# Optimization experiments

Measured on AMD Instinct MI355X. Metric: run time of the kernel, lower is better.

The kernel has to match this reference:

```python
import jax, jax.numpy as jnp
import numpy as np

EMBED = 768
HEADS = 12
HEAD_DIM = EMBED // HEADS
HIDDEN = 3072
EPS = 1e-5


def setup_inputs() -> dict:
    key = jax.random.key(0)
    ks = jax.random.split(key, 8)
    s = lambda d: 1.0 / np.sqrt(d)
    return {
        "x": jax.random.normal(ks[0], (1, 4096, EMBED), jnp.float32),
        "ln1_w": jnp.ones((EMBED,), jnp.float32),
        "ln1_b": jnp.zeros((EMBED,), jnp.float32),
        "qkv_w": jax.random.normal(ks[1], (3 * EMBED, EMBED), jnp.float32) * s(EMBED),
        "qkv_b": jnp.zeros((3 * EMBED,), jnp.float32),
        "out_w": jax.random.normal(ks[2], (EMBED, EMBED), jnp.float32) * s(EMBED),
        "out_b": jnp.zeros((EMBED,), jnp.float32),
        "ln2_w": jnp.ones((EMBED,), jnp.float32),
        "ln2_b": jnp.zeros((EMBED,), jnp.float32),
        "fc1_w": jax.random.normal(ks[3], (HIDDEN, EMBED), jnp.float32) * s(EMBED),
        "fc1_b": jnp.zeros((HIDDEN,), jnp.float32),
        "fc2_w": jax.random.normal(ks[4], (EMBED, HIDDEN), jnp.float32) * s(HIDDEN),
        "fc2_b": jnp.zeros((EMBED,), jnp.float32),
    }


def _layernorm(x, w, b):
    mu = jnp.mean(x, axis=-1, keepdims=True)
    var = jnp.mean(jnp.square(x - mu), axis=-1, keepdims=True)
    return (x - mu) * jax.lax.rsqrt(var + EPS) * w + b


def reference(x, ln1_w, ln1_b, qkv_w, qkv_b, out_w, out_b,
              ln2_w, ln2_b, fc1_w, fc1_b, fc2_w, fc2_b):
    B, N, _ = x.shape
    # attention branch
    h = _layernorm(x, ln1_w, ln1_b)
    qkv = h @ qkv_w.T + qkv_b                      # [B,N,3E]
    qkv = qkv.reshape(B, N, 3, HEADS, HEAD_DIM)
    q = jnp.transpose(qkv[:, :, 0], (0, 2, 1, 3))  # [B,H,N,D]
    k = jnp.transpose(qkv[:, :, 1], (0, 2, 1, 3))
    v = jnp.transpose(qkv[:, :, 2], (0, 2, 1, 3))
    scores = jnp.einsum("bhqd,bhkd->bhqk", q, k) / np.sqrt(HEAD_DIM)
    probs = jax.nn.softmax(scores, axis=-1)
    attn = jnp.einsum("bhqk,bhkd->bhqd", probs, v)
    attn = jnp.transpose(attn, (0, 2, 1, 3)).reshape(B, N, EMBED)
    x = x + (attn @ out_w.T + out_b)
    # mlp branch
    h = _layernorm(x, ln2_w, ln2_b)
    h = jax.nn.gelu(h @ fc1_w.T + fc1_b, approximate=False)
    x = x + (h @ fc2_w.T + fc2_b)
    return x
```

## Files before the change

kernel.cpp:

```cpp
#include <hip/hip_runtime.h>
#include <hip/hip_bf16.h>

#define SEQ  4096
#define EMB  768
#define NH   12
#define HD   64
#define HID  3072
#define QKVC 2304

typedef __attribute__((ext_vector_type(8))) short bf16x8;
typedef __attribute__((ext_vector_type(4))) float f32x4;

#define MFMA16(a,b,c) __builtin_amdgcn_mfma_f32_16x16x32_bf16(a,b,c,0,0,0)

#define QSCL 0.18033688f

__device__ __forceinline__ unsigned short f2bf(float f){
  union { float f; unsigned u; } c; c.f = f;
  unsigned r = c.u + 0x7FFFu + ((c.u >> 16) & 1u);
  return (unsigned short)(r >> 16);
}

__device__ __forceinline__ float bf2f(unsigned short u){
  union { unsigned u; float f; } c; c.u = (unsigned)u << 16; return c.f;
}

__device__ __forceinline__ unsigned cvtpk(float a, float b){
  unsigned r;
  asm("v_cvt_pk_bf16_f32 %0, %1, %2" : "=v"(r) : "v"(a), "v"(b));
  return r;
}

__device__ __forceinline__ void gload_lds16(const unsigned short* g, unsigned short* l){
  __builtin_amdgcn_global_load_lds(
      (const __attribute__((address_space(1))) unsigned int*)g,
      (__attribute__((address_space(3))) unsigned int*)l, 16, 0, 0);
}

__global__ void cvt4_kernel(const float* __restrict__ s0, unsigned short* __restrict__ d0, int n0,
                            const float* __restrict__ s1, unsigned short* __restrict__ d1, int n1,
                            const float* __restrict__ s2, unsigned short* __restrict__ d2, int n2,
                            const float* __restrict__ s3, unsigned short* __restrict__ d3, int n3){
  long e = ((long)blockIdx.x * 256 + threadIdx.x) << 2;
  const float* s; unsigned short* d;
  if (e < n0){ s = s0; d = d0; }
  else if ((e -= n0) < n1){ s = s1; d = d1; }
  else if ((e -= n1) < n2){ s = s2; d = d2; }
  else if ((e -= n2) < n3){ s = s3; d = d3; }
  else return;
  float4 v = *(const float4*)(s + e);
  ushort4 u;
  u.x = f2bf(v.x); u.y = f2bf(v.y); u.z = f2bf(v.z); u.w = f2bf(v.w);
  *(ushort4*)(d + e) = u;
}

__global__ __launch_bounds__(256) void ln_kernel(const float* __restrict__ x,
    const float* __restrict__ w, const float* __restrict__ b,
    unsigned short* __restrict__ out)
{
  const int row = blockIdx.x;
  const float* xr = x + (size_t)row * EMB;
  const int t = threadIdx.x;
  float v0 = xr[t], v1 = xr[t + 256], v2 = xr[t + 512];
  float s  = v0 + v1 + v2;
  float s2 = v0*v0 + v1*v1 + v2*v2;
  #pragma unroll
  for (int off = 32; off; off >>= 1){ s += __shfl_down(s, off); s2 += __shfl_down(s2, off); }
  __shared__ float rs[4], rq[4], st[2];
  int wv = t >> 6;
  if ((t & 63) == 0){ rs[wv] = s; rq[wv] = s2; }
  __syncthreads();
  if (t == 0){
    float S  = rs[0] + rs[1] + rs[2] + rs[3];
    float S2 = rq[0] + rq[1] + rq[2] + rq[3];
    float mu  = S * (1.f / 768.f);
    float var = S2 * (1.f / 768.f) - mu * mu;
    st[0] = mu; st[1] = rsqrtf(var + 1e-5f);
  }
  __syncthreads();
  float mu = st[0], rstd = st[1];
  unsigned short* orow = out + (size_t)row * EMB;
  orow[t]       = f2bf((v0 - mu) * rstd * w[t]       + b[t]);
  orow[t + 256] = f2bf((v1 - mu) * rstd * w[t + 256] + b[t + 256]);
  orow[t + 512] = f2bf((v2 - mu) * rstd * w[t + 512] + b[t + 512]);
}

template<int EPI, int BM, int BN, int DBUF>
__global__ __launch_bounds__(256, 3) void gemm_kernel(
    const unsigned short* __restrict__ A, const unsigned short* __restrict__ B,
    const float* __restrict__ bias, const float* __restrict__ res,
    unsigned short* __restrict__ Ob, float* __restrict__ Of,
    int M, int N, int K)
{
  constexpr int MF = BM / 32;
  constexpr int NF = BN / 32;
  constexpr int NB = DBUF ? 2 : 1;
  __shared__ unsigned short sA[NB][BM * 64];
  __shared__ unsigned short sB[NB][BN * 64];
  const int tid  = threadIdx.x;
  const int w    = tid >> 6, lane = tid & 63;
  const int wr   = w >> 1,   wc   = w & 1;
  const int l15  = lane & 15, l4  = lane >> 4;
  const int tm   = blockIdx.y, tn = blockIdx.x;
  const unsigned short* Ab = A + (size_t)tm * BM * K;
  const unsigned short* Bb = B + (size_t)tn * BN * K;

  f32x4 acc[MF][NF];
  #pragma unroll
  for (int m = 0; m < MF; ++m)
    #pragma unroll
    for (int n = 0; n < NF; ++n){ acc[m][n][0]=0.f; acc[m][n][1]=0.f; acc[m][n][2]=0.f; acc[m][n][3]=0.f; }

  #define GSTAGE(buf, kt) { \
    const int k0_ = (kt) << 6; \
    _Pragma("unroll") \
    for (int i = 0; i < MF; ++i){ \
      int c = i * 256 + tid; int row = c >> 3; int skc = (c & 7) ^ (row & 7); \
      gload_lds16(Ab + (size_t)row * K + k0_ + skc * 8, &sA[buf][(i * 256 + w * 64) * 8]); } \
    _Pragma("unroll") \
    for (int i = 0; i < NF; ++i){ \
      int c = i * 256 + tid; int row = c >> 3; int skc = (c & 7) ^ (row & 7); \
      gload_lds16(Bb + (size_t)row * K + k0_ + skc * 8, &sB[buf][(i * 256 + w * 64) * 8]); }}

  #define GCOMPUTE(buf) { \
    _Pragma("unroll") \
    for (int ks = 0; ks < 2; ++ks){ \
      bf16x8 af[MF], bg[NF]; \
      _Pragma("unroll") \
      for (int m = 0; m < MF; ++m){ \
        int row = wr * (BM / 2) + m * 16 + l15; \
        int kc  = ks * 4 + l4; \
        af[m] = *(const bf16x8*)&sA[buf][row * 64 + ((kc ^ (row & 7)) << 3)]; } \
      _Pragma("unroll") \
      for (int n = 0; n < NF; ++n){ \
        int row = wc * (BN / 2) + n * 16 + l15; \
        int kc  = ks * 4 + l4; \
        bg[n] = *(const bf16x8*)&sB[buf][row * 64 + ((kc ^ (row & 7)) << 3)]; } \
      _Pragma("unroll") \
      for (int m = 0; m < MF; ++m) \
        _Pragma("unroll") \
        for (int n = 0; n < NF; ++n) \
          acc[m][n] = MFMA16(af[m], bg[n], acc[m][n]); }}

  const int nk = K >> 6;
  if (DBUF){
    GSTAGE(0, 0);
    int cur = 0;
    for (int kt = 0; kt < nk; ++kt){
      __syncthreads();
      if (kt + 1 < nk) GSTAGE(cur ^ 1, kt + 1);
      GCOMPUTE(cur % NB);
      cur ^= 1;
    }
  } else {
    for (int kt = 0; kt < nk; ++kt){
      GSTAGE(0, kt);
      __syncthreads();
      GCOMPUTE(0);
      __syncthreads();
    }
  }
  #undef GSTAGE
  #undef GCOMPUTE

  #pragma unroll
  for (int m = 0; m < MF; ++m){
    int row0 = tm * BM + wr * (BM / 2) + m * 16 + l4 * 4;
    #pragma unroll
    for (int n = 0; n < NF; ++n){
      int col = tn * BN + wc * (BN / 2) + n * 16 + l15;
      float bv = bias[col];
      #pragma unroll
      for (int r = 0; r < 4; ++r){
        int row = row0 + r;
        float v = acc[m][n][r] + bv;
        if (EPI == 0){
          Ob[(size_t)row * N + col] = f2bf(v);
        } else if (EPI == 1){
          v = 0.5f * v * (1.f + erff(v * 0.70710678118f));
          Ob[(size_t)row * N + col] = f2bf(v);
        } else if (EPI == 3){
          if (col < EMB) v *= QSCL;
          Ob[(size_t)row * N + col] = f2bf(v);
        } else {
          v += res[(size_t)row * N + col];
          Of[(size_t)row * N + col] = v;
        }
      }
    }
  }
}

__global__ __launch_bounds__(256, 3) void attn_kernel(
    const unsigned short* __restrict__ qkv,
    unsigned short* __restrict__ pO, float2* __restrict__ pml)
{
  __shared__ unsigned short sK[2][64 * 64];
  __shared__ unsigned short sVt[2][64 * 64];
  __shared__ unsigned short sEp[4][16 * 72];
  const int tid = threadIdx.x, w = tid >> 6, lane = tid & 63;
  const int l15 = lane & 15, l4 = lane >> 4;

  const int bid  = blockIdx.x;
  const int v_id = (bid & 7) * 96 + (bid >> 3);
  const int head = v_id >> 6;
  const int r6   = v_id & 63;
  const int qt   = r6 >> 1;
  const int sk   = r6 & 1;

  const int koff = EMB + head * HD;
  const int voff = 2 * EMB + head * HD;
  const int qbase = qt * 128 + w * 32;
  const int tbase = sk * 32;

  bf16x8 qf[2][2];
  #pragma unroll
  for (int qg = 0; qg < 2; ++qg){
    const unsigned short* qp = qkv + (size_t)(qbase + qg * 16 + l15) * QKVC + head * HD + l4 * 8;
    qf[qg][0] = *(const bf16x8*)qp;
    qf[qg][1] = *(const bf16x8*)(qp + 32);
  }

  f32x4 oaccT[4][2];
  #pragma unroll
  for (int i = 0; i < 4; ++i)
    #pragma unroll
    for (int qg = 0; qg < 2; ++qg){ oaccT[i][qg][0]=0.f; oaccT[i][qg][1]=0.f; oaccT[i][qg][2]=0.f; oaccT[i][qg][3]=0.f; }
  float m0 = -3.0e38f, m1 = -3.0e38f, l0 = 0.f, l1 = 0.f;

  const int krow = tid >> 3;
  const int kskc = (tid & 7) ^ (krow & 7);
  const int vp_  = tid >> 3;
  const int d0   = (tid & 7) * 8;
  const int w16  = vp_ & 15;
  const int qpos = (w16 & 1) | (((w16 >> 3) & 1) << 1) | (((w16 >> 1) & 3) << 2);
  const int Pc   = ((vp_ >> 4) << 2) | (qpos >> 2);
  const int Ps   = qpos & 3;

  #define KSTAGE(buf, t) { \
    const int kv0_ = (t) << 6; \
    gload_lds16(qkv + (size_t)(kv0_ + krow) * QKVC + koff + kskc * 8,      &sK[buf][(w * 64) * 8]); \
    gload_lds16(qkv + (size_t)(kv0_ + 32 + krow) * QKVC + koff + kskc * 8, &sK[buf][(256 + w * 64) * 8]); }

  #define VLOAD(t) { \
    const unsigned short* vp = qkv + (size_t)(((t) << 6) + vp_ * 2) * QKVC + voff + d0; \
    va = *(const bf16x8*)vp; \
    vb = *(const bf16x8*)(vp + QKVC); }

  #define VCOMMIT(buf) { \
    _Pragma("unroll") \
    for (int i = 0; i < 8; ++i){ \
      unsigned pk = (unsigned)(unsigned short)va[i] | ((unsigned)(unsigned short)vb[i] << 16); \
      *(unsigned*)&sVt[buf][(d0 + i) * 64 + ((Pc ^ (tid & 7) ^ i) << 3) + Ps * 2] = pk; \
    } }

  bf16x8 va, vb;
  KSTAGE(0, tbase);
  VLOAD(tbase);
  VCOMMIT(0);

  for (int tt = 0; tt < 32; ++tt){
    const int cur = tt & 1;
    __syncthreads();
    const bool pre = (tt < 31);
    if (pre){
      KSTAGE(cur ^ 1, tbase + tt + 1);
      VLOAD(tbase + tt + 1);
    }

    f32x4 sf[4][2];
    #pragma unroll
    for (int i = 0; i < 4; ++i)
      #pragma unroll
      for (int qg = 0; qg < 2; ++qg){ sf[i][qg][0]=0.f; sf[i][qg][1]=0.f; sf[i][qg][2]=0.f; sf[i][qg][3]=0.f; }
    __builtin_amdgcn_s_setprio(1);
    #pragma unroll
    for (int ks = 0; ks < 2; ++ks){
      bf16x8 kf[4];
      #pragma unroll
      for (int nb = 0; nb < 4; ++nb){
        int row = 16 * nb + l15;
        kf[nb] = *(const bf16x8*)&sK[cur][(row * 8 + ((4 * ks + l4) ^ (row & 7))) * 8];
      }
      #pragma unroll
      for (int nb = 0; nb < 4; ++nb){
        sf[nb][0] = MFMA16(kf[nb], qf[0][ks], sf[nb][0]);
        sf[nb][1] = MFMA16(kf[nb], qf[1][ks], sf[nb][1]);
      }
    }
    __builtin_amdgcn_s_setprio(0);

    float mx0, mx1;
    {
      float a = sf[0][0][0], b = sf[0][1][0];
      #pragma unroll
      for (int nb = 0; nb < 4; ++nb)
        #pragma unroll
        for (int r = 0; r < 4; ++r){
          a = fmaxf(a, sf[nb][0][r]);
          b = fmaxf(b, sf[nb][1][r]);
        }
      a = fmaxf(a, __shfl_xor(a, 16)); a = fmaxf(a, __shfl_xor(a, 32));
      b = fmaxf(b, __shfl_xor(b, 16)); b = fmaxf(b, __shfl_xor(b, 32));
      mx0 = a; mx1 = b;
    }
    bool ok = (mx0 <= m0 + 8.f) && (mx1 <= m1 + 8.f);
    if (!__all(ok)){
      float nm0 = fmaxf(m0, mx0), nm1 = fmaxf(m1, mx1);
      float c0 = __builtin_amdgcn_exp2f(m0 - nm0);
      float c1 = __builtin_amdgcn_exp2f(m1 - nm1);
      m0 = nm0; m1 = nm1; l0 *= c0; l1 *= c1;
      #pragma unroll
      for (int db = 0; db < 4; ++db)
        #pragma unroll
        for (int r = 0; r < 4; ++r){ oaccT[db][0][r] *= c0; oaccT[db][1][r] *= c1; }
    }
    unsigned pbw[2][2][4];
    {
      float ps0 = 0.f, ps1 = 0.f;
      #pragma unroll
      for (int nb = 0; nb < 4; ++nb){
        float p0[4], p1[4];
        #pragma unroll
        for (int r = 0; r < 4; ++r){
          p0[r] = __builtin_amdgcn_exp2f(sf[nb][0][r] - m0); ps0 += p0[r];
          p1[r] = __builtin_amdgcn_exp2f(sf[nb][1][r] - m1); ps1 += p1[r];
        }
        pbw[0][nb >> 1][(nb & 1) * 2]     = cvtpk(p0[0], p0[1]);
        pbw[0][nb >> 1][(nb & 1) * 2 + 1] = cvtpk(p0[2], p0[3]);
        pbw[1][nb >> 1][(nb & 1) * 2]     = cvtpk(p1[0], p1[1]);
        pbw[1][nb >> 1][(nb & 1) * 2 + 1] = cvtpk(p1[2], p1[3]);
      }
      ps0 += __shfl_xor(ps0, 16); ps0 += __shfl_xor(ps0, 32);
      ps1 += __shfl_xor(ps1, 16); ps1 += __shfl_xor(ps1, 32);
      l0 += ps0; l1 += ps1;
    }

    __builtin_amdgcn_s_setprio(1);
    {
      bf16x8 vv[2][4];
      #pragma unroll
      for (int ks = 0; ks < 2; ++ks)
        #pragma unroll
        for (int db = 0; db < 4; ++db){
          int d = 16 * db + l15;
          int cp = (4 * ks + l4) ^ ((d >> 3) & 7) ^ (d & 7);
          vv[ks][db] = *(const bf16x8*)&sVt[cur][d * 64 + cp * 8];
        }
      union { unsigned uw[4]; bf16x8 v; } pb;
      #pragma unroll
      for (int qg = 0; qg < 2; ++qg){
        bf16x8 pb0, pb1;
        pb.uw[0]=pbw[qg][0][0]; pb.uw[1]=pbw[qg][0][1]; pb.uw[2]=pbw[qg][0][2]; pb.uw[3]=pbw[qg][0][3]; pb0 = pb.v;
        pb.uw[0]=pbw[qg][1][0]; pb.uw[1]=pbw[qg][1][1]; pb.uw[2]=pbw[qg][1][2]; pb.uw[3]=pbw[qg][1][3]; pb1 = pb.v;
        #pragma unroll
        for (int db = 0; db < 4; ++db){
          oaccT[db][qg] = MFMA16(vv[0][db], pb0, oaccT[db][qg]);
          oaccT[db][qg] = MFMA16(vv[1][db], pb1, oaccT[db][qg]);
        }
      }
    }
    __builtin_amdgcn_s_setprio(0);

    if (pre) VCOMMIT(cur ^ 1);
  }

  #pragma unroll
  for (int qg = 0; qg < 2; ++qg){
    unsigned short* sPw = sEp[w];
    #pragma unroll
    for (int db = 0; db < 4; ++db)
      #pragma unroll
      for (int dw = 0; dw < 2; ++dw){
        unsigned pk = cvtpk(oaccT[db][qg][2 * dw], oaccT[db][qg][2 * dw + 1]);
        *(unsigned*)&sPw[l15 * 72 + 16 * db + 4 * l4 + 2 * dw] = pk;
      }
    int qe = lane >> 2, de = (lane & 3) * 16;
    bf16x8 r0 = *(const bf16x8*)&sPw[qe * 72 + de];
    bf16x8 r1 = *(const bf16x8*)&sPw[qe * 72 + de + 8];
    unsigned short* op = pO + ((size_t)(sk * NH + head) * SEQ + qbase + qg * 16 + qe) * 64 + de;
    *(bf16x8*)op = r0;
    *(bf16x8*)(op + 8) = r1;
  }
  if (lane < 16){
    size_t r = (size_t)(sk * NH + head) * SEQ + qbase + l15;
    pml[r]      = make_float2(m0, l0);
    pml[r + 16] = make_float2(m1, l1);
  }
  #undef KSTAGE
  #undef VLOAD
  #undef VCOMMIT
}

__global__ __launch_bounds__(256) void comb_kernel(
    const unsigned short* __restrict__ pO, const float2* __restrict__ pml,
    unsigned short* __restrict__ o)
{
  const int t = threadIdx.x;
  const int row = blockIdx.x * 64 + (t >> 2);
  const int dseg = (t & 3) * 16;
  float2 a = pml[row], b = pml[NH * SEQ + row];
  float M = fmaxf(a.x, b.x);
  float c0 = __builtin_amdgcn_exp2f(a.x - M);
  float c1 = __builtin_amdgcn_exp2f(b.x - M);
  float inv = 1.f / (c0 * a.y + c1 * b.y);
  c0 *= inv; c1 *= inv;
  const unsigned short* p0 = pO + (size_t)row * 64 + dseg;
  const unsigned short* p1 = p0 + (size_t)NH * SEQ * 64;
  bf16x8 x0 = *(const bf16x8*)p0, x1 = *(const bf16x8*)(p0 + 8);
  bf16x8 y0 = *(const bf16x8*)p1, y1 = *(const bf16x8*)(p1 + 8);
  const int head = row >> 12, q = row & (SEQ - 1);
  unsigned short* op = o + (size_t)q * EMB + head * HD + dseg;
  union { unsigned uw[4]; bf16x8 v; } r0, r1;
  #pragma unroll
  for (int i = 0; i < 4; ++i){
    r0.uw[i] = cvtpk(c0 * bf2f((unsigned short)x0[2*i])   + c1 * bf2f((unsigned short)y0[2*i]),
                     c0 * bf2f((unsigned short)x0[2*i+1]) + c1 * bf2f((unsigned short)y0[2*i+1]));
    r1.uw[i] = cvtpk(c0 * bf2f((unsigned short)x1[2*i])   + c1 * bf2f((unsigned short)y1[2*i]),
                     c0 * bf2f((unsigned short)x1[2*i+1]) + c1 * bf2f((unsigned short)y1[2*i+1]));
  }
  *(bf16x8*)op = r0.v;
  *(bf16x8*)(op + 8) = r1.v;
}

extern "C" void kernel_launch(void* const* d_in, const int* in_sizes, int n_in,
                              void* d_out, int out_size, void* d_ws, size_t ws_size,
                              hipStream_t stream)
{
  const float* x    = (const float*)d_in[0];
  const float* ln1w = (const float*)d_in[1];
  const float* ln1b = (const float*)d_in[2];
  const float* qkvw = (const float*)d_in[3];
  const float* qkvb = (const float*)d_in[4];
  const float* outw = (const float*)d_in[5];
  const float* outb = (const float*)d_in[6];
  const float* ln2w = (const float*)d_in[7];
  const float* ln2b = (const float*)d_in[8];
  const float* fc1w = (const float*)d_in[9];
  const float* fc1b = (const float*)d_in[10];
  const float* fc2w = (const float*)d_in[11];
  const float* fc2b = (const float*)d_in[12];
  float* out = (float*)d_out;

  char* ws = (char*)d_ws;
  unsigned short* wqkv = (unsigned short*)ws; ws += (size_t)QKVC * EMB * 2;
  unsigned short* wout = (unsigned short*)ws; ws += (size_t)EMB * EMB * 2;
  unsigned short* wfc1 = (unsigned short*)ws; ws += (size_t)HID * EMB * 2;
  unsigned short* wfc2 = (unsigned short*)ws; ws += (size_t)EMB * HID * 2;
  unsigned short* h1   = (unsigned short*)ws; ws += (size_t)SEQ * EMB * 2;
  unsigned short* qkv  = (unsigned short*)ws; ws += (size_t)SEQ * QKVC * 2;
  unsigned short* h3   = (unsigned short*)ws; ws += (size_t)SEQ * HID * 2;
  unsigned short* attnb = h1;
  unsigned short* h2    = qkv;
  unsigned short* pO  = h3;
  float2*         pml = (float2*)(h3 + (size_t)2 * NH * SEQ * 64);

  const int n0 = QKVC * EMB, n1 = EMB * EMB, n2 = HID * EMB, n3 = EMB * HID;
  cvt4_kernel<<<(n0 + n1 + n2 + n3) / 4 / 256, 256, 0, stream>>>(
      qkvw, wqkv, n0, outw, wout, n1, fc1w, wfc1, n2, fc2w, wfc2, n3);

  ln_kernel<<<SEQ, 256, 0, stream>>>(x, ln1w, ln1b, h1);

  gemm_kernel<3, 128, 128, 0><<<dim3(QKVC / 128, SEQ / 128), 256, 0, stream>>>(
      h1, wqkv, qkvb, nullptr, qkv, nullptr, SEQ, QKVC, EMB);

  attn_kernel<<<SEQ / 128 * NH * 2, 256, 0, stream>>>(qkv, pO, pml);
  comb_kernel<<<NH * SEQ / 64, 256, 0, stream>>>(pO, pml, attnb);

  gemm_kernel<2, 64, 64, 1><<<dim3(EMB / 64, SEQ / 64), 256, 0, stream>>>(
      attnb, wout, outb, x, nullptr, out, SEQ, EMB, EMB);

  ln_kernel<<<SEQ, 256, 0, stream>>>(out, ln2w, ln2b, h2);

  gemm_kernel<1, 128, 128, 0><<<dim3(HID / 128, SEQ / 128), 256, 0, stream>>>(
      h2, wfc1, fc1b, nullptr, h3, nullptr, SEQ, HID, EMB);

  gemm_kernel<2, 64, 64, 1><<<dim3(EMB / 64, SEQ / 64), 256, 0, stream>>>(
      h3, wfc2, fc2b, out, nullptr, out, SEQ, EMB, HID);
}
```

Before: 214.2 us.

## Double-buffer all GEMMs with templated K-tile and use fast sigmoid-form GELU

The GEMM kernel now takes the K-tile size as a template parameter and always double-buffers its shared-memory stages. The 128x128 QKV and FC1 GEMMs move from single-buffered BK=64 to double-buffered BK=32, keeping roughly the same LDS footprint while overlapping global-to-LDS loads with MFMA work. The 64x64 GEMMs get a higher occupancy hint in their launch bounds. The erf-based GELU epilogue is replaced with an exp2/rcp sigmoid-form tanh approximation, which is cheaper but differs slightly from exact GELU.

```diff
diff --git a/kernel.cpp b/kernel.cpp
--- a/kernel.cpp
+++ b/kernel.cpp
@@ -29,6 +29,12 @@
   unsigned r;
   asm("v_cvt_pk_bf16_f32 %0, %1, %2" : "=v"(r) : "v"(a), "v"(b));
   return r;
+}
+
+__device__ __forceinline__ float gelu_f(float x){
+  float x2 = x * x;
+  float u  = __builtin_amdgcn_exp2f(x * fmaf(x2, 0.1029433f, 2.3022082f));
+  return x * u * __builtin_amdgcn_rcpf(1.f + u);
 }
 
 __device__ __forceinline__ void gload_lds16(const unsigned short* g, unsigned short* l){
@@ -85,18 +91,21 @@
   orow[t + 512] = f2bf((v2 - mu) * rstd * w[t + 512] + b[t + 512]);
 }
 
-template<int EPI, int BM, int BN, int DBUF>
-__global__ __launch_bounds__(256, 3) void gemm_kernel(
+template<int EPI, int BM, int BN, int BK>
+__global__ __launch_bounds__(256, (BM == 64 ? 4 : 3)) void gemm_kernel(
     const unsigned short* __restrict__ A, const unsigned short* __restrict__ B,
     const float* __restrict__ bias, const float* __restrict__ res,
     unsigned short* __restrict__ Ob, float* __restrict__ Of,
     int M, int N, int K)
 {
-  constexpr int MF = BM / 32;
-  constexpr int NF = BN / 32;
-  constexpr int NB = DBUF ? 2 : 1;
-  __shared__ unsigned short sA[NB][BM * 64];
-  __shared__ unsigned short sB[NB][BN * 64];
+  constexpr int MF  = BM / 32;
+  constexpr int NF  = BN / 32;
+  constexpr int KS  = BK / 32;
+  constexpr int CPR = BK / 8;
+  constexpr int AIT = BM * BK / 2048;
+  constexpr int BIT = BN * BK / 2048;
+  __shared__ unsigned short sA[2][BM * BK];
+  __shared__ unsigned short sB[2][BN * BK];
   const int tid  = threadIdx.x;
   const int w    = tid >> 6, lane = tid & 63;
   const int wr   = w >> 1,   wc   = w & 1;
@@ -112,53 +121,44 @@
     for (int n = 0; n < NF; ++n){ acc[m][n][0]=0.f; acc[m][n][1]=0.f; acc[m][n][2]=0.f; acc[m][n][3]=0.f; }
 
   #define GSTAGE(buf, kt) { \
-    const int k0_ = (kt) << 6; \
+    const int k0_ = (kt) * BK; \
     _Pragma("unroll") \
-    for (int i = 0; i < MF; ++i){ \
-      int c = i * 256 + tid; int row = c >> 3; int skc = (c & 7) ^ (row & 7); \
+    for (int i = 0; i < AIT; ++i){ \
+      int c = i * 256 + tid; int row = c / CPR; int skc = (c % CPR) ^ (row & (CPR - 1)); \
       gload_lds16(Ab + (size_t)row * K + k0_ + skc * 8, &sA[buf][(i * 256 + w * 64) * 8]); } \
     _Pragma("unroll") \
-    for (int i = 0; i < NF; ++i){ \
-      int c = i * 256 + tid; int row = c >> 3; int skc = (c & 7) ^ (row & 7); \
+    for (int i = 0; i < BIT; ++i){ \
+      int c = i * 256 + tid; int row = c / CPR; int skc = (c % CPR) ^ (row & (CPR - 1)); \
       gload_lds16(Bb + (size_t)row * K + k0_ + skc * 8, &sB[buf][(i * 256 + w * 64) * 8]); }}
 
   #define GCOMPUTE(buf) { \
     _Pragma("unroll") \
-    for (int ks = 0; ks < 2; ++ks){ \
+    for (int ks = 0; ks < KS; ++ks){ \
       bf16x8 af[MF], bg[NF]; \
       _Pragma("unroll") \
       for (int m = 0; m < MF; ++m){ \
         int row = wr * (BM / 2) + m * 16 + l15; \
         int kc  = ks * 4 + l4; \
-        af[m] = *(const bf16x8*)&sA[buf][row * 64 + ((kc ^ (row & 7)) << 3)]; } \
+        af[m] = *(const bf16x8*)&sA[buf][row * BK + ((kc ^ (row & (CPR - 1))) << 3)]; } \
       _Pragma("unroll") \
       for (int n = 0; n < NF; ++n){ \
         int row = wc * (BN / 2) + n * 16 + l15; \
         int kc  = ks * 4 + l4; \
-        bg[n] = *(const bf16x8*)&sB[buf][row * 64 + ((kc ^ (row & 7)) << 3)]; } \
+        bg[n] = *(const bf16x8*)&sB[buf][row * BK + ((kc ^ (row & (CPR - 1))) << 3)]; } \
       _Pragma("unroll") \
       for (int m = 0; m < MF; ++m) \
         _Pragma("unroll") \
         for (int n = 0; n < NF; ++n) \
           acc[m][n] = MFMA16(af[m], bg[n], acc[m][n]); }}
 
-  const int nk = K >> 6;
-  if (DBUF){
-    GSTAGE(0, 0);
-    int cur = 0;
-    for (int kt = 0; kt < nk; ++kt){
-      __syncthreads();
-      if (kt + 1 < nk) GSTAGE(cur ^ 1, kt + 1);
-      GCOMPUTE(cur % NB);
-      cur ^= 1;
-    }
-  } else {
-    for (int kt = 0; kt < nk; ++kt){
-      GSTAGE(0, kt);
-      __syncthreads();
-      GCOMPUTE(0);
-      __syncthreads();
-    }
+  const int nk = K / BK;
+  GSTAGE(0, 0);
+  int cur = 0;
+  for (int kt = 0; kt < nk; ++kt){
+    __syncthreads();
+    if (kt + 1 < nk) GSTAGE(cur ^ 1, kt + 1);
+    GCOMPUTE(cur);
+    cur ^= 1;
   }
   #undef GSTAGE
   #undef GCOMPUTE
@@ -177,8 +177,7 @@
         if (EPI == 0){
           Ob[(size_t)row * N + col] = f2bf(v);
         } else if (EPI == 1){
-          v = 0.5f * v * (1.f + erff(v * 0.70710678118f));
-          Ob[(size_t)row * N + col] = f2bf(v);
+          Ob[(size_t)row * N + col] = f2bf(gelu_f(v));
         } else if (EPI == 3){
           if (col < EMB) v *= QSCL;
           Ob[(size_t)row * N + col] = f2bf(v);
@@ -461,20 +460,20 @@
 
   ln_kernel<<<SEQ, 256, 0, stream>>>(x, ln1w, ln1b, h1);
 
-  gemm_kernel<3, 128, 128, 0><<<dim3(QKVC / 128, SEQ / 128), 256, 0, stream>>>(
+  gemm_kernel<3, 128, 128, 32><<<dim3(QKVC / 128, SEQ / 128), 256, 0, stream>>>(
       h1, wqkv, qkvb, nullptr, qkv, nullptr, SEQ, QKVC, EMB);
 
   attn_kernel<<<SEQ / 128 * NH * 2, 256, 0, stream>>>(qkv, pO, pml);
   comb_kernel<<<NH * SEQ / 64, 256, 0, stream>>>(pO, pml, attnb);
 
-  gemm_kernel<2, 64, 64, 1><<<dim3(EMB / 64, SEQ / 64), 256, 0, stream>>>(
+  gemm_kernel<2, 64, 64, 64><<<dim3(EMB / 64, SEQ / 64), 256, 0, stream>>>(
       attnb, wout, outb, x, nullptr, out, SEQ, EMB, EMB);
 
   ln_kernel<<<SEQ, 256, 0, stream>>>(out, ln2w, ln2b, h2);
 
-  gemm_kernel<1, 128, 128, 0><<<dim3(HID / 128, SEQ / 128), 256, 0, stream>>>(
+  gemm_kernel<1, 128, 128, 32><<<dim3(HID / 128, SEQ / 128), 256, 0, stream>>>(
       h2, wfc1, fc1b, nullptr, h3, nullptr, SEQ, HID, EMB);
 
-  gemm_kernel<2, 64, 64, 1><<<dim3(EMB / 64, SEQ / 64), 256, 0, stream>>>(
+  gemm_kernel<2, 64, 64, 64><<<dim3(EMB / 64, SEQ / 64), 256, 0, stream>>>(
       h3, wfc2, fc2b, out, nullptr, out, SEQ, EMB, HID);
 }
```

Result: no change. 210.4 us (-1.7%).
